# Kernel tuning notes

Hardware: AMD Instinct MI355X
Metric: run time of the kernel (lower is better)

## Reference

```python
import jax, jax.numpy as jnp
import numpy as np

N_STATE = 64
D_MODEL = 128


def setup_inputs() -> dict:
    key = jax.random.key(0)
    k1, k2, k3 = jax.random.split(key, 3)
    # Matches torch init: A = diag(rand(N)), B = rand(N, d_model), C = rand(d_model, N)
    A = jnp.diag(jax.random.uniform(k1, (N_STATE,), dtype=jnp.float32))
    B = jax.random.uniform(k2, (N_STATE, D_MODEL), dtype=jnp.float32)
    C = jax.random.uniform(k3, (D_MODEL, N_STATE), dtype=jnp.float32)
    return {"A": A, "B": B, "C": C, "L": 4096}


def reference(A, B, C, L):
    # K[i] = C @ A^i @ B, i = 0..L-1.
    # Instead of L independent matrix_power calls (O(L * N^3)), carry
    # P_i = C @ A^i  (d_model, N) through a scan: P_{i+1} = P_i @ A.
    def step(P, _):
        K_i = P @ B            # (d_model, d_model)
        return P @ A, K_i

    _, K = jax.lax.scan(step, C, None, length=L)
    return K  # (L, d_model, d_model)
```

## Files before the change

kernel.cpp:

```cpp
#include <hip/hip_runtime.h>
#include <math.h>

#define D_MODEL 128
#define N_STATE 64
#define SEQ_L   4096
#define CHUNK   8
#define GRID    (SEQ_L / CHUNK)

typedef __attribute__((ext_vector_type(8))) __bf16 bf16x8;
typedef __attribute__((ext_vector_type(4))) float  f32x4;

__global__ __launch_bounds__(256, 2) void s4d_mfma_kernel(
    const float* __restrict__ A,
    const float* __restrict__ B,
    const float* __restrict__ C,
    float* __restrict__ K)
{
    const int tid  = threadIdx.x;
    const int w    = tid >> 6;
    const int lane = tid & 63;
    const int ln   = lane & 15;
    const int q    = lane >> 4;
    const int i0   = blockIdx.x * CHUNK;

    float avec[2][8], Csval[2][2][8];
    #pragma unroll
    for (int s = 0; s < 2; ++s)
        #pragma unroll
        for (int j = 0; j < 8; ++j) {
            const int k = 32*s + 8*q + j;
            const float a = A[k * N_STATE + k];
            avec[s][j] = a;
            const float p = powf(a, (float)i0);
            #pragma unroll
            for (int t = 0; t < 2; ++t)
                Csval[t][s][j] = C[(32*w + 16*t + ln) * N_STATE + k] * p;
        }

    bf16x8 Bfrag[8][2];
    #pragma unroll
    for (int c = 0; c < 8; ++c)
        #pragma unroll
        for (int s = 0; s < 2; ++s) {
            bf16x8 f;
            #pragma unroll
            for (int j = 0; j < 8; ++j)
                f[j] = (__bf16)B[(32*s + 8*q + j) * D_MODEL + 16*c + ln];
            Bfrag[c][s] = f;
        }

    float* out = K + (size_t)i0 * (D_MODEL * D_MODEL);

    for (int i = 0; i < CHUNK; ++i) {
        bf16x8 Cfrag[2][2];
        #pragma unroll
        for (int t = 0; t < 2; ++t)
            #pragma unroll
            for (int s = 0; s < 2; ++s) {
                bf16x8 f;
                #pragma unroll
                for (int j = 0; j < 8; ++j)
                    f[j] = (__bf16)Csval[t][s][j];
                Cfrag[t][s] = f;
            }

        f32x4 acc[2][8];
        #pragma unroll
        for (int t = 0; t < 2; ++t)
            #pragma unroll
            for (int c = 0; c < 8; ++c) {
                f32x4 z = {0.f, 0.f, 0.f, 0.f};
                f32x4 d = __builtin_amdgcn_mfma_f32_16x16x32_bf16(
                    Bfrag[c][0], Cfrag[t][0], z, 0, 0, 0);
                d = __builtin_amdgcn_mfma_f32_16x16x32_bf16(
                    Bfrag[c][1], Cfrag[t][1], d, 0, 0, 0);
                acc[t][c] = d;
            }

        #pragma unroll
        for (int t = 0; t < 2; ++t) {
            float* rowp = out + (32*w + 16*t + ln) * D_MODEL + 4*q;
            #pragma unroll
            for (int c = 0; c < 8; ++c) {
                float4 v = make_float4(acc[t][c][0], acc[t][c][1],
                                       acc[t][c][2], acc[t][c][3]);
                *(float4*)(rowp + 16*c) = v;
            }
        }

        #pragma unroll
        for (int t = 0; t < 2; ++t)
            #pragma unroll
            for (int s = 0; s < 2; ++s)
                #pragma unroll
                for (int j = 0; j < 8; ++j)
                    Csval[t][s][j] *= avec[s][j];

        out += D_MODEL * D_MODEL;
    }
}

extern "C" void kernel_launch(void* const* d_in, const int* in_sizes, int n_in,
                              void* d_out, int out_size, void* d_ws, size_t ws_size,
                              hipStream_t stream) {
    const float* A = (const float*)d_in[0];
    const float* B = (const float*)d_in[1];
    const float* C = (const float*)d_in[2];
    float* K = (float*)d_out;
    s4d_mfma_kernel<<<dim3(GRID), dim3(256), 0, stream>>>(A, B, C, K);
}
```

Measured before the change: 265.8 us.

## Stage B fragments in swizzled LDS and shrink chunk to raise occupancy

```diff
diff --git a/kernel.cpp b/kernel.cpp
--- a/kernel.cpp
+++ b/kernel.cpp
@@ -4,24 +4,34 @@
 #define D_MODEL 128
 #define N_STATE 64
 #define SEQ_L   4096
-#define CHUNK   8
+#define CHUNK   2
 #define GRID    (SEQ_L / CHUNK)
 
 typedef __attribute__((ext_vector_type(8))) __bf16 bf16x8;
 typedef __attribute__((ext_vector_type(4))) float  f32x4;
 
-__global__ __launch_bounds__(256, 2) void s4d_mfma_kernel(
+__global__ __launch_bounds__(256, 4) void s4d_mfma_kernel(
     const float* __restrict__ A,
     const float* __restrict__ B,
     const float* __restrict__ C,
     float* __restrict__ K)
 {
+    __shared__ __align__(16) __bf16 Blds[N_STATE * D_MODEL];
+
     const int tid  = threadIdx.x;
     const int w    = tid >> 6;
     const int lane = tid & 63;
     const int ln   = lane & 15;
     const int q    = lane >> 4;
     const int i0   = blockIdx.x * CHUNK;
+
+    for (int e = tid; e < N_STATE * D_MODEL; e += 256) {
+        const int row = e >> 7;
+        const int col = e & 127;
+        const int rb  = row >> 3;
+        const int p16 = col * 8 + (rb ^ (col & 7));
+        Blds[p16 * 8 + (row & 7)] = (__bf16)B[row * D_MODEL + col];
+    }
 
     float avec[2][8], Csval[2][2][8];
     #pragma unroll
@@ -37,54 +47,36 @@
                 Csval[t][s][j] = C[(32*w + 16*t + ln) * N_STATE + k] * p;
         }
 
-    bf16x8 Bfrag[8][2];
-    #pragma unroll
-    for (int c = 0; c < 8; ++c)
-        #pragma unroll
-        for (int s = 0; s < 2; ++s) {
-            bf16x8 f;
-            #pragma unroll
-            for (int j = 0; j < 8; ++j)
-                f[j] = (__bf16)B[(32*s + 8*q + j) * D_MODEL + 16*c + ln];
-            Bfrag[c][s] = f;
-        }
+    __syncthreads();
+
+    const int addr_s0 = (8*ln + ( q      ^ (ln & 7))) * 16;
+    const int addr_s1 = (8*ln + ((4 + q) ^ (ln & 7))) * 16;
+    const char* ldsb = (const char*)Blds;
 
     float* out = K + (size_t)i0 * (D_MODEL * D_MODEL);
 
     for (int i = 0; i < CHUNK; ++i) {
-        bf16x8 Cfrag[2][2];
-        #pragma unroll
-        for (int t = 0; t < 2; ++t)
-            #pragma unroll
-            for (int s = 0; s < 2; ++s) {
-                bf16x8 f;
-                #pragma unroll
-                for (int j = 0; j < 8; ++j)
-                    f[j] = (__bf16)Csval[t][s][j];
-                Cfrag[t][s] = f;
-            }
-
-        f32x4 acc[2][8];
-        #pragma unroll
-        for (int t = 0; t < 2; ++t)
-            #pragma unroll
-            for (int c = 0; c < 8; ++c) {
-                f32x4 z = {0.f, 0.f, 0.f, 0.f};
-                f32x4 d = __builtin_amdgcn_mfma_f32_16x16x32_bf16(
-                    Bfrag[c][0], Cfrag[t][0], z, 0, 0, 0);
-                d = __builtin_amdgcn_mfma_f32_16x16x32_bf16(
-                    Bfrag[c][1], Cfrag[t][1], d, 0, 0, 0);
-                acc[t][c] = d;
-            }
-
         #pragma unroll
         for (int t = 0; t < 2; ++t) {
+            bf16x8 cf0, cf1;
+            #pragma unroll
+            for (int j = 0; j < 8; ++j) {
+                cf0[j] = (__bf16)Csval[t][0][j];
+                cf1[j] = (__bf16)Csval[t][1][j];
+            }
             float* rowp = out + (32*w + 16*t + ln) * D_MODEL + 4*q;
             #pragma unroll
             for (int c = 0; c < 8; ++c) {
-                float4 v = make_float4(acc[t][c][0], acc[t][c][1],
-                                       acc[t][c][2], acc[t][c][3]);
-                *(float4*)(rowp + 16*c) = v;
+                const bf16x8 b0 =
+                    *reinterpret_cast<const bf16x8*>(ldsb + addr_s0 + 2048*c);
+                const bf16x8 b1 =
+                    *reinterpret_cast<const bf16x8*>(ldsb + addr_s1 + 2048*c);
+                f32x4 z = {0.f, 0.f, 0.f, 0.f};
+                f32x4 d = __builtin_amdgcn_mfma_f32_16x16x32_bf16(
+                    b0, cf0, z, 0, 0, 0);
+                d = __builtin_amdgcn_mfma_f32_16x16x32_bf16(
+                    b1, cf1, d, 0, 0, 0);
+                *(float4*)(rowp + 16*c) = make_float4(d[0], d[1], d[2], d[3]);
             }
         }
 
```

After: 283.3 us. +6.6%, slower.
